# Performance work log

Hardware: AMD Instinct MI355X
Metric: run time of the kernel (lower is better)

## Reference

```python
import jax, jax.numpy as jnp
import numpy as np

N_NODES = 100000
N_EDGES = 1600000
N_GRAPHS = 512


def _graph_conv(x, W, b, src, dst, n_nodes):
    """DGL GraphConv, norm='both': D_in^-1/2 (A (D_out^-1/2 x)) W + b.
    Weight is applied on the smaller-dim side (same math, less memory)."""
    ones = jnp.ones(src.shape[0], dtype=x.dtype)
    deg_out = jnp.clip(jax.ops.segment_sum(ones, src, num_segments=n_nodes), 1.0)
    deg_in = jnp.clip(jax.ops.segment_sum(ones, dst, num_segments=n_nodes), 1.0)
    h = x * (deg_out ** -0.5)[:, None]
    if W.shape[0] > W.shape[1]:  # reduce feature dim before the SpMM
        h = h @ W
        h = jax.ops.segment_sum(h[src], dst, num_segments=n_nodes)
    else:
        h = jax.ops.segment_sum(h[src], dst, num_segments=n_nodes)
        h = h @ W
    return h * (deg_in ** -0.5)[:, None] + b


def setup_inputs() -> dict:
    key = jax.random.key(0)
    ks = jax.random.split(key, 16)
    x = jax.random.normal(ks[0], (N_NODES, 128), dtype=jnp.float32)
    src = jax.random.randint(ks[1], (N_EDGES,), 0, N_NODES, dtype=jnp.int32)
    dst = jax.random.randint(ks[2], (N_EDGES,), 0, N_NODES, dtype=jnp.int32)
    graph_ids = jnp.sort(jax.random.randint(ks[3], (N_NODES,), 0, N_GRAPHS, dtype=jnp.int32))
    s = 0.05
    return {
        "x": x, "src": src, "dst": dst, "graph_ids": graph_ids,
        "W1": jax.random.normal(ks[4], (128, 256), jnp.float32) * s,
        "b1": jnp.zeros((256,), jnp.float32),
        "W2": jax.random.normal(ks[5], (256, 64), jnp.float32) * s,
        "b2": jnp.zeros((64,), jnp.float32),
        "Wc1": jax.random.normal(ks[6], (64, 18), jnp.float32) * s,
        "bc1": jnp.zeros((18,), jnp.float32),
        "Wc2": jax.random.normal(ks[7], (18, 12), jnp.float32) * s,
        "bc2": jnp.zeros((12,), jnp.float32),
        "Wc3": jax.random.normal(ks[8], (12, 6), jnp.float32) * s,
        "bc3": jnp.zeros((6,), jnp.float32),
        "Wc4": jax.random.normal(ks[9], (6, 2), jnp.float32) * s,
        "bc4": jnp.zeros((2,), jnp.float32),
    }


def reference(x, src, dst, graph_ids, W1, b1, W2, b2, Wc1, bc1, Wc2, bc2, Wc3, bc3, Wc4, bc4):
    n = x.shape[0]
    h = jax.nn.relu(_graph_conv(x, W1, b1, src, dst, n))
    h = jax.nn.relu(_graph_conv(h, W2, b2, src, dst, n))
    # dgl.mean_nodes: per-graph mean over nodes
    sums = jax.ops.segment_sum(h, graph_ids, num_segments=N_GRAPHS)
    cnts = jnp.clip(jax.ops.segment_sum(jnp.ones(n, h.dtype), graph_ids, num_segments=N_GRAPHS), 1.0)
    hg = sums / cnts[:, None]
    # classifier: 4 stacked Linear layers, no activations (faithful to source)
    hg = hg @ Wc1 + bc1
    hg = hg @ Wc2 + bc2
    hg = hg @ Wc3 + bc3
    return hg @ Wc4 + bc4
```

## Files before the change

kernel.cpp:

```cpp
#include <hip/hip_runtime.h>
#include <cstdint>
#include <cstddef>

#define NGRAPHS 512

static inline size_t align_up(size_t x, size_t a){ return (x + a - 1) & ~(a - 1); }

__device__ __forceinline__ unsigned short f2bf(float f){
  unsigned int u = __float_as_uint(f);
  u += 0x7FFFu + ((u >> 16) & 1u);
  return (unsigned short)(u >> 16);
}
__device__ __forceinline__ float bflo(unsigned int u){ return __uint_as_float(u << 16); }
__device__ __forceinline__ float bfhi(unsigned int u){ return __uint_as_float(u & 0xffff0000u); }
__device__ __forceinline__ unsigned int pack2(float a, float b){
  return (unsigned)f2bf(a) | ((unsigned)f2bf(b) << 16);
}

typedef __attribute__((ext_vector_type(8))) short bf16x8;
typedef __attribute__((ext_vector_type(4))) float f32x4;

__global__ __launch_bounds__(256) void k_partcount(const int* __restrict__ src, const int* __restrict__ dst,
                                                   int* __restrict__ cntS, int* __restrict__ cntD, int n_edges, int NBLK,
                                                   const float* __restrict__ W1, unsigned short* __restrict__ Wt1,
                                                   const float* __restrict__ W2, unsigned short* __restrict__ Wt2,
                                                   const int* __restrict__ gids, int* __restrict__ gb, int n_nodes){
  __shared__ int cs[256], cd[256];
  if (blockIdx.x >= NBLK){
    long long u = (long long)(blockIdx.x - NBLK) * 256 + threadIdx.x;
    if (u < 128 * 256){
      int k = (int)(u / 256), n = (int)(u % 256);
      Wt1[(size_t)n * 128 + k] = f2bf(W1[u]);
      return;
    }
    u -= 128 * 256;
    if (u < 256 * 64){
      int k = (int)(u / 64), n = (int)(u % 64);
      Wt2[(size_t)n * 256 + k] = f2bf(W2[u]);
      return;
    }
    u -= 256 * 64;
    if (u < n_nodes){
      int i = (int)u;
      int g  = gids[i];
      int gp = (i > 0) ? gids[i - 1] : -1;
      for (int q = gp + 1; q <= g; ++q) gb[q] = i;
      if (i == n_nodes - 1)
        for (int q = g + 1; q <= NGRAPHS; ++q) gb[q] = n_nodes;
    }
    return;
  }
  int tid = threadIdx.x;
  cs[tid] = 0; cd[tid] = 0;
  __syncthreads();
  int e0 = blockIdx.x * 4096;
  int e1 = min(e0 + 4096, n_edges);
  for (int e = e0 + tid; e < e1; e += 256){
    atomicAdd(&cs[src[e] >> 9], 1);
    atomicAdd(&cd[dst[e] >> 9], 1);
  }
  __syncthreads();
  cntS[blockIdx.x * 256 + tid] = cs[tid];
  cntD[blockIdx.x * 256 + tid] = cd[tid];
}

__global__ __launch_bounds__(256) void k_colscan(int* __restrict__ cntS, int* __restrict__ cntD,
                                                 int* __restrict__ totS, int* __restrict__ totD,
                                                 int nblk, int NB){
  int col = blockIdx.x;
  int* cnt; int* tot; int k;
  if (col < NB){ cnt = cntS; tot = totS; k = col; }
  else         { cnt = cntD; tot = totD; k = col - NB; }
  __shared__ int tsum[256];
  int tid = threadIdx.x;
  int i0 = 2 * tid, i1 = 2 * tid + 1;
  int a = (i0 < nblk) ? cnt[i0 * 256 + k] : 0;
  int b = (i1 < nblk) ? cnt[i1 * 256 + k] : 0;
  int s = a + b;
  tsum[tid] = s;
  __syncthreads();
  for (int off = 1; off < 256; off <<= 1){
    int t = (tid >= off) ? tsum[tid - off] : 0;
    __syncthreads();
    tsum[tid] += t;
    __syncthreads();
  }
  int pre = tsum[tid] - s;
  if (i0 < nblk) cnt[i0 * 256 + k] = pre;
  if (i1 < nblk) cnt[i1 * 256 + k] = pre + a;
  if (tid == 255) tot[k] = tsum[255];
}

__global__ __launch_bounds__(256) void k_scatter_det(const int* __restrict__ src, const int* __restrict__ dst,
                                                     const int* __restrict__ cntS, const int* __restrict__ cntD,
                                                     const int* __restrict__ totS, const int* __restrict__ totD,
                                                     int* __restrict__ baseS, int* __restrict__ baseD,
                                                     int2* __restrict__ pairD, int* __restrict__ srcS,
                                                     int n_edges, int NB){
  __shared__ int s1[256], s2[256];
  __shared__ int gbS[256], gbD[256], lsS[256], lsD[256], lcS[256], lcD[256];
  __shared__ int2 ebuf[4096];
  __shared__ int sbuf[4096];
  int tid = threadIdx.x;
  int b = blockIdx.x;
  int v1 = (tid < NB) ? totS[tid] : 0;
  int v2 = (tid < NB) ? totD[tid] : 0;
  s1[tid] = v1; s2[tid] = v2;
  __syncthreads();
  for (int off = 1; off < 256; off <<= 1){
    int t1 = (tid >= off) ? s1[tid - off] : 0;
    int t2 = (tid >= off) ? s2[tid - off] : 0;
    __syncthreads();
    s1[tid] += t1; s2[tid] += t2;
    __syncthreads();
  }
  int bS = s1[tid] - v1, bD = s2[tid] - v2;
  if (b == 0 && tid < NB){ baseS[tid] = bS; baseD[tid] = bD; }
  gbS[tid] = bS + cntS[b * 256 + tid];
  gbD[tid] = bD + cntD[b * 256 + tid];
  __syncthreads();
  int e0 = b * 4096, e1 = min(e0 + 4096, n_edges);
  int ne = e1 - e0;
  s1[tid] = 0; s2[tid] = 0;
  __syncthreads();
  for (int e = e0 + tid; e < e1; e += 256){
    atomicAdd(&s1[src[e] >> 9], 1);
    atomicAdd(&s2[dst[e] >> 9], 1);
  }
  __syncthreads();
  int hv1 = s1[tid], hv2 = s2[tid];
  __syncthreads();
  s1[tid] = hv1; s2[tid] = hv2;
  __syncthreads();
  for (int off = 1; off < 256; off <<= 1){
    int t1 = (tid >= off) ? s1[tid - off] : 0;
    int t2 = (tid >= off) ? s2[tid - off] : 0;
    __syncthreads();
    s1[tid] += t1; s2[tid] += t2;
    __syncthreads();
  }
  lsS[tid] = s1[tid] - hv1; lcS[tid] = lsS[tid];
  lsD[tid] = s2[tid] - hv2; lcD[tid] = lsD[tid];
  __syncthreads();
  for (int e = e0 + tid; e < e1; e += 256){
    int sv = src[e], d = dst[e];
    int lp = atomicAdd(&lcD[d >> 9], 1);
    ebuf[lp] = make_int2(sv, d);
    int sp = atomicAdd(&lcS[sv >> 9], 1);
    sbuf[sp] = sv;
  }
  __syncthreads();
  for (int i = tid; i < ne; i += 256){
    int2 e = ebuf[i];
    int kd = e.y >> 9;
    pairD[gbD[kd] + i - lsD[kd]] = e;
    int sv = sbuf[i];
    int ks = sv >> 9;
    srcS[gbS[ks] + i - lsS[ks]] = sv;
  }
}

__global__ __launch_bounds__(256) void k_bucket_build(const int2* __restrict__ pairD, const int* __restrict__ baseD,
                                                      const int* __restrict__ srcS, const int* __restrict__ baseS,
                                                      int* __restrict__ offs, float* __restrict__ din_s,
                                                      float* __restrict__ dout_s, int* __restrict__ csr_src,
                                                      int NB, int n, int n_edges){
  __shared__ int cnt[512], cur[512];
  __shared__ int tsum[256];
  int tid = threadIdx.x;
  int bb = blockIdx.x;
  bool dstSide = bb < NB;
  int b = dstSide ? bb : bb - NB;
  int node0 = b << 9;
  int nn = min(512, n - node0);
  for (int i = tid; i < 512; i += 256) cnt[i] = 0;
  __syncthreads();
  if (dstSide){
    int jd0 = baseD[b], jd1 = (b + 1 < NB) ? baseD[b + 1] : n_edges;
    for (int j = jd0 + tid; j < jd1; j += 256) atomicAdd(&cnt[pairD[j].y - node0], 1);
    __syncthreads();
    int a0 = cnt[2 * tid], a1 = cnt[2 * tid + 1];
    int s = a0 + a1;
    tsum[tid] = s;
    __syncthreads();
    for (int off = 1; off < 256; off <<= 1){
      int t = (tid >= off) ? tsum[tid - off] : 0;
      __syncthreads();
      tsum[tid] += t;
      __syncthreads();
    }
    int pre = tsum[tid] - s + jd0;
    cur[2 * tid]     = pre;
    cur[2 * tid + 1] = pre + a0;
    __syncthreads();
    for (int i = tid; i < nn; i += 256){
      offs[node0 + i]  = cur[i];
      din_s[node0 + i] = 1.0f / sqrtf((float)max(cnt[i], 1));
    }
    if (b == NB - 1 && tid == 0) offs[n] = n_edges;
    __syncthreads();
    for (int j = jd0 + tid; j < jd1; j += 256){
      int2 e = pairD[j];
      int p = atomicAdd(&cur[e.y - node0], 1);
      csr_src[p] = e.x;
    }
  } else {
    int js0 = baseS[b], js1 = (b + 1 < NB) ? baseS[b + 1] : n_edges;
    for (int j = js0 + tid; j < js1; j += 256) atomicAdd(&cnt[srcS[j] - node0], 1);
    __syncthreads();
    for (int i = tid; i < nn; i += 256)
      dout_s[node0 + i] = 1.0f / sqrtf((float)max(cnt[i], 1));
  }
}

__global__ __launch_bounds__(256) void k_prep2(const float* __restrict__ x,
                                               const float* __restrict__ dout_s,
                                               unsigned int* __restrict__ xb, long long total4){
  long long t = (long long)blockIdx.x * 256 + threadIdx.x;
  if (t >= total4) return;
  float4 v = ((const float4*)x)[t];
  float s = dout_s[t >> 5];
  xb[t * 2 + 0] = pack2(v.x * s, v.y * s);
  xb[t * 2 + 1] = pack2(v.z * s, v.w * s);
}

__global__ __launch_bounds__(256) void k_spmm1(const unsigned int* __restrict__ xb,
    const int* __restrict__ offs, const int* __restrict__ csr_src,
    unsigned int* __restrict__ aggb, int n_nodes){
  int node = __builtin_amdgcn_readfirstlane((int)((blockIdx.x * 256u + threadIdx.x) >> 6));
  if (node >= n_nodes) return;
  int lane = threadIdx.x & 63;
  int j0 = offs[node], j1 = offs[node + 1];
  float ax = 0.f, ay = 0.f;
  int j = j0;
  for (; j + 4 <= j1; j += 4){
    int s0 = csr_src[j + 0];
    int s1 = csr_src[j + 1];
    int s2 = csr_src[j + 2];
    int s3 = csr_src[j + 3];
    unsigned v0 = xb[(size_t)s0 * 64 + lane];
    unsigned v1 = xb[(size_t)s1 * 64 + lane];
    unsigned v2 = xb[(size_t)s2 * 64 + lane];
    unsigned v3 = xb[(size_t)s3 * 64 + lane];
    ax += bflo(v0) + bflo(v1) + bflo(v2) + bflo(v3);
    ay += bfhi(v0) + bfhi(v1) + bfhi(v2) + bfhi(v3);
  }
  for (; j < j1; ++j){
    unsigned v = xb[(size_t)csr_src[j] * 64 + lane];
    ax += bflo(v);
    ay += bfhi(v);
  }
  aggb[(size_t)node * 64 + lane] = pack2(ax, ay);
}

__global__ __launch_bounds__(256) void k_gemm12(const unsigned short* __restrict__ A,
    const unsigned short* __restrict__ Bt, const unsigned short* __restrict__ Wt2,
    unsigned short* __restrict__ T2,
    int M, const float* __restrict__ din, const float* __restrict__ dout,
    const float* __restrict__ bias){
  constexpr int LDA = 136;
  constexpr int LDH = 72;
  __shared__ __align__(16) unsigned short As[128 * LDA];
  __shared__ __align__(16) unsigned short Bs[64 * LDA];
  __shared__ __align__(16) unsigned short Hs[128 * LDH];
  int tid = threadIdx.x;
  int bm0 = blockIdx.x * 128;
  int wid = tid >> 6, lane = tid & 63;
  int wm = wid * 32;
  int quad = lane >> 4, l16 = lane & 15;

  uint4 areg[8];
#pragma unroll
  for (int it = 0; it < 8; ++it){
    int i = tid + it * 256;
    int m = i >> 4, c = i & 15;
    int gr = bm0 + m;
    areg[it] = (gr < M) ? *(const uint4*)(A + (size_t)gr * 128 + c * 8) : make_uint4(0u, 0u, 0u, 0u);
  }
  uint4 breg[4];
#pragma unroll
  for (int it = 0; it < 4; ++it){
    int i = tid + it * 256;
    int n = i >> 4, c = i & 15;
    breg[it] = *(const uint4*)(Bt + (size_t)n * 128 + c * 8);
  }
#pragma unroll
  for (int it = 0; it < 8; ++it){
    int i = tid + it * 256;
    int m = i >> 4, c = i & 15;
    *(uint4*)&As[m * LDA + c * 8] = areg[it];
  }
#pragma unroll
  for (int it = 0; it < 4; ++it){
    int i = tid + it * 256;
    int n = i >> 4, c = i & 15;
    *(uint4*)&Bs[n * LDA + c * 8] = breg[it];
  }
  float rsv[2][4], rs2v[2][4];
#pragma unroll
  for (int t = 0; t < 2; ++t)
#pragma unroll
    for (int r = 0; r < 4; ++r){
      int gr = bm0 + wm + t * 16 + quad * 4 + r;
      rsv[t][r]  = (gr < M) ? din[gr]  : 0.f;
      rs2v[t][r] = (gr < M) ? dout[gr] : 0.f;
    }
  f32x4 tacc[2][4];
#pragma unroll
  for (int t = 0; t < 2; ++t)
#pragma unroll
    for (int u = 0; u < 4; ++u) tacc[t][u] = f32x4{0.f, 0.f, 0.f, 0.f};
  __syncthreads();

  for (int nt = 0; nt < 4; ++nt){
    if (nt < 3){
#pragma unroll
      for (int it = 0; it < 4; ++it){
        int i = tid + it * 256;
        int n = i >> 4, c = i & 15;
        breg[it] = *(const uint4*)(Bt + (size_t)((nt + 1) * 64 + n) * 128 + c * 8);
      }
    }
    f32x4 acc[2][4];
#pragma unroll
    for (int t = 0; t < 2; ++t)
#pragma unroll
      for (int u = 0; u < 4; ++u) acc[t][u] = f32x4{0.f, 0.f, 0.f, 0.f};
#pragma unroll
    for (int ks = 0; ks < 4; ++ks){
      bf16x8 af[2], bfr[4];
#pragma unroll
      for (int t = 0; t < 2; ++t)
        af[t] = *(const bf16x8*)&As[(wm + t * 16 + l16) * LDA + ks * 32 + quad * 8];
#pragma unroll
      for (int u = 0; u < 4; ++u)
        bfr[u] = *(const bf16x8*)&Bs[(u * 16 + l16) * LDA + ks * 32 + quad * 8];
#pragma unroll
      for (int t = 0; t < 2; ++t)
#pragma unroll
        for (int u = 0; u < 4; ++u)
          acc[t][u] = __builtin_amdgcn_mfma_f32_16x16x32_bf16(af[t], bfr[u], acc[t][u], 0, 0, 0);
    }
    float bv[4];
#pragma unroll
    for (int u = 0; u < 4; ++u) bv[u] = bias[nt * 64 + u * 16 + l16];
#pragma unroll
    for (int t = 0; t < 2; ++t)
#pragma unroll
      for (int r = 0; r < 4; ++r){
        int row = wm + t * 16 + quad * 4 + r;
#pragma unroll
        for (int u = 0; u < 4; ++u){
          float cv = fmaxf(fmaf(acc[t][u][r], rsv[t][r], bv[u]), 0.f) * rs2v[t][r];
          Hs[row * LDH + u * 16 + l16] = f2bf(cv);
        }
      }
    __syncthreads();
#pragma unroll
    for (int ks2 = 0; ks2 < 2; ++ks2){
      bf16x8 haf[2], wbf[4];
#pragma unroll
      for (int t = 0; t < 2; ++t)
        haf[t] = *(const bf16x8*)&Hs[(wm + t * 16 + l16) * LDH + ks2 * 32 + quad * 8];
#pragma unroll
      for (int u = 0; u < 4; ++u)
        wbf[u] = *(const bf16x8*)(Wt2 + (size_t)(u * 16 + l16) * 256 + nt * 64 + ks2 * 32 + quad * 8);
#pragma unroll
      for (int t = 0; t < 2; ++t)
#pragma unroll
        for (int u = 0; u < 4; ++u)
          tacc[t][u] = __builtin_amdgcn_mfma_f32_16x16x32_bf16(haf[t], wbf[u], tacc[t][u], 0, 0, 0);
    }
    __syncthreads();
    if (nt < 3){
#pragma unroll
      for (int it = 0; it < 4; ++it){
        int i = tid + it * 256;
        int n = i >> 4, c = i & 15;
        *(uint4*)&Bs[n * LDA + c * 8] = breg[it];
      }
      __syncthreads();
    }
  }
#pragma unroll
  for (int t = 0; t < 2; ++t)
#pragma unroll
    for (int r = 0; r < 4; ++r){
      int gr = bm0 + wm + t * 16 + quad * 4 + r;
      if (gr < M){
#pragma unroll
        for (int u = 0; u < 4; ++u)
          T2[(size_t)gr * 64 + u * 16 + l16] = f2bf(tacc[t][u][r]);
      }
    }
}

#define SCHUNK 4
__global__ __launch_bounds__(256) void k_spmm2_fused(const unsigned short* __restrict__ t2,
    const int* __restrict__ offs, const int* __restrict__ csr_src,
    const float* __restrict__ din_s, const float* __restrict__ b2,
    const int* __restrict__ gb, float* __restrict__ sums){
  __shared__ float bs[64];
  int tid = threadIdx.x;
  int g = blockIdx.x & (NGRAPHS - 1);
  int chunk = blockIdx.x >> 9;
  int wW = __builtin_amdgcn_readfirstlane(chunk * 4 + (tid >> 6));
  int lane = tid & 63, half = lane >> 5, l = lane & 31;
  if (tid < 64) bs[tid] = 0.f;
  __syncthreads();
  int g0 = gb[g], g1 = gb[g + 1];
  const unsigned int* tp = (const unsigned int*)t2;
  float2 bb = ((const float2*)b2)[l];
  float gxs = 0.f, gys = 0.f;
  for (int node = g0 + wW; node < g1; node += 16){
    int j0 = offs[node], j1 = offs[node + 1];
    float ax = 0.f, ay = 0.f;
    int j = j0;
    for (; j + 2 <= j1; j += 2){
      int s0 = csr_src[j], s1 = csr_src[j + 1];
      int ss = half ? s1 : s0;
      unsigned v = tp[(size_t)ss * 32 + l];
      ax += bflo(v);
      ay += bfhi(v);
    }
    if (j < j1 && half == 0){
      unsigned v = tp[(size_t)csr_src[j] * 32 + l];
      ax += bflo(v);
      ay += bfhi(v);
    }
    ax += __shfl_xor(ax, 32);
    ay += __shfl_xor(ay, 32);
    float ds = din_s[node];
    gxs += fmaxf(fmaf(ax, ds, bb.x), 0.f);
    gys += fmaxf(fmaf(ay, ds, bb.y), 0.f);
  }
  if (half == 0){
    atomicAdd(&bs[2 * l], gxs);
    atomicAdd(&bs[2 * l + 1], gys);
  }
  __syncthreads();
  if (tid < 64) atomicAdd(&sums[(size_t)g * 64 + tid], bs[tid]);
}

__global__ __launch_bounds__(256) void k_classifier(const float* __restrict__ sums, const int* __restrict__ gb,
    const float* __restrict__ Wc1, const float* __restrict__ bc1,
    const float* __restrict__ Wc2, const float* __restrict__ bc2,
    const float* __restrict__ Wc3, const float* __restrict__ bc3,
    const float* __restrict__ Wc4, const float* __restrict__ bc4,
    float* __restrict__ out){
  __shared__ float w1[64 * 18], w2[18 * 12], w3[12 * 6], w4[6 * 2];
  __shared__ float B1[18], B2[12], B3[6], B4[2];
  int tid = threadIdx.x;
  for (int i = tid; i < 64 * 18; i += 256) w1[i] = Wc1[i];
  for (int i = tid; i < 18 * 12; i += 256) w2[i] = Wc2[i];
  for (int i = tid; i < 12 * 6;  i += 256) w3[i] = Wc3[i];
  for (int i = tid; i < 6 * 2;   i += 256) w4[i] = Wc4[i];
  if (tid < 18) B1[tid] = bc1[tid];
  if (tid < 12) B2[tid] = bc2[tid];
  if (tid < 6)  B3[tid] = bc3[tid];
  if (tid < 2)  B4[tid] = bc4[tid];
  __syncthreads();
  int g = blockIdx.x * 256 + tid;
  float cnt = fmaxf((float)(gb[g + 1] - gb[g]), 1.0f);
  float h[64];
#pragma unroll
  for (int f = 0; f < 64; ++f) h[f] = sums[(size_t)g * 64 + f] / cnt;
  float t1[18];
#pragma unroll
  for (int j = 0; j < 18; ++j){
    float s = B1[j];
    for (int f = 0; f < 64; ++f) s = fmaf(h[f], w1[f * 18 + j], s);
    t1[j] = s;
  }
  float t2[12];
#pragma unroll
  for (int j = 0; j < 12; ++j){
    float s = B2[j];
    for (int f = 0; f < 18; ++f) s = fmaf(t1[f], w2[f * 12 + j], s);
    t2[j] = s;
  }
  float t3[6];
#pragma unroll
  for (int j = 0; j < 6; ++j){
    float s = B3[j];
    for (int f = 0; f < 12; ++f) s = fmaf(t2[f], w3[f * 6 + j], s);
    t3[j] = s;
  }
#pragma unroll
  for (int j = 0; j < 2; ++j){
    float s = B4[j];
    for (int f = 0; f < 6; ++f) s = fmaf(t3[f], w4[f * 2 + j], s);
    out[(size_t)g * 2 + j] = s;
  }
}

extern "C" void kernel_launch(void* const* d_in, const int* in_sizes, int n_in,
                              void* d_out, int out_size, void* d_ws, size_t ws_size,
                              hipStream_t stream){
  const float* x   = (const float*)d_in[0];
  const int*   src = (const int*)d_in[1];
  const int*   dst = (const int*)d_in[2];
  const int*   gid = (const int*)d_in[3];
  const float* W1  = (const float*)d_in[4];
  const float* b1  = (const float*)d_in[5];
  const float* W2  = (const float*)d_in[6];
  const float* b2  = (const float*)d_in[7];
  const float* Wc1 = (const float*)d_in[8];
  const float* bc1 = (const float*)d_in[9];
  const float* Wc2 = (const float*)d_in[10];
  const float* bc2 = (const float*)d_in[11];
  const float* Wc3 = (const float*)d_in[12];
  const float* bc3 = (const float*)d_in[13];
  const float* Wc4 = (const float*)d_in[14];
  const float* bc4 = (const float*)d_in[15];
  float* out = (float*)d_out;

  const int n_nodes = in_sizes[3];
  const int n_edges = in_sizes[1];
  const int F1 = 256, F2 = 64;
  const int NB   = (n_nodes + 511) >> 9;
  const int NBLK = (n_edges + 4095) / 4096;

  char* w = (char*)d_ws;
  size_t o = 0;
  auto alloc = [&](size_t bytes) -> char* {
    char* p = w + o;
    o = align_up(o + bytes, 256);
    return p;
  };
  float* sums      = (float*)alloc((size_t)NGRAPHS * F2 * 4);
  int*   gb        = (int*)  alloc((size_t)(NGRAPHS + 1) * 4);
  int*   cntS      = (int*)  alloc((size_t)NBLK * 256 * 4);
  int*   cntD      = (int*)  alloc((size_t)NBLK * 256 * 4);
  int*   totS      = (int*)  alloc((size_t)256 * 4);
  int*   totD      = (int*)  alloc((size_t)256 * 4);
  int*   baseS     = (int*)  alloc((size_t)256 * 4);
  int*   baseD     = (int*)  alloc((size_t)256 * 4);
  float* dout_s    = (float*)alloc((size_t)n_nodes * 4);
  float* din_s     = (float*)alloc((size_t)n_nodes * 4);
  int*   offs      = (int*)  alloc((size_t)(n_nodes + 1) * 4);
  int*   csr_src   = (int*)  alloc((size_t)n_edges * 4);
  unsigned short* Wt1 = (unsigned short*)alloc((size_t)256 * 128 * 2);
  unsigned short* Wt2 = (unsigned short*)alloc((size_t)64 * 256 * 2);
  unsigned int*   xb  = (unsigned int*)  alloc((size_t)n_nodes * 128 * 2);
  unsigned short* aggb= (unsigned short*)alloc((size_t)n_nodes * 128 * 2);
  unsigned short* h1b = (unsigned short*)alloc((size_t)n_nodes * F1 * 2);
  int2*  pairD = (int2*)aggb;
  int*   srcS  = (int*)((char*)aggb + (size_t)n_edges * 8);
  unsigned short* t2b = h1b;

  hipMemsetAsync(sums, 0, (size_t)NGRAPHS * F2 * 4, stream);

  {
    long long miscTotal = 128 * 256 + 256 * 64 + n_nodes;
    int miscBlocks = (int)((miscTotal + 255) / 256);
    k_partcount<<<NBLK + miscBlocks, 256, 0, stream>>>(src, dst, cntS, cntD, n_edges, NBLK,
                                                       W1, Wt1, W2, Wt2, gid, gb, n_nodes);
  }
  k_colscan     <<<2 * NB, 256, 0, stream>>>(cntS, cntD, totS, totD, NBLK, NB);
  k_scatter_det <<<NBLK, 256, 0, stream>>>(src, dst, cntS, cntD, totS, totD, baseS, baseD, pairD, srcS, n_edges, NB);
  k_bucket_build<<<2 * NB, 256, 0, stream>>>(pairD, baseD, srcS, baseS, offs, din_s, dout_s, csr_src,
                                             NB, n_nodes, n_edges);

  {
    long long total4 = (long long)n_nodes * 32;
    k_prep2<<<(int)((total4 + 255) / 256), 256, 0, stream>>>(x, dout_s, xb, total4);
  }

  int gx = (n_nodes + 127) / 128;
  {
    long long threads = (long long)n_nodes * 64;
    k_spmm1<<<(int)((threads + 255) / 256), 256, 0, stream>>>(xb, offs, csr_src, (unsigned int*)aggb, n_nodes);
    k_gemm12<<<gx, 256, 0, stream>>>(aggb, Wt1, Wt2, t2b, n_nodes, din_s, dout_s, b1);
  }
  k_spmm2_fused<<<NGRAPHS * SCHUNK, 256, 0, stream>>>(t2b, offs, csr_src, din_s, b2, gb, sums);
  k_classifier<<<NGRAPHS / 256, 256, 0, stream>>>(sums, gb, Wc1, bc1, Wc2, bc2, Wc3, bc3, Wc4, bc4, out);
}
```

Before: 345.2 us.

## Fuse layer-1 SpMM gather into the GEMM kernel and unroll layer-2 gather

The layer-1 neighbor aggregation now runs inside the GEMM kernel. Each wave gathers its own 32 rows, two nodes interleaved, straight into LDS, so the aggregated bf16 intermediate is never written to or re-read from global memory. The W1 tile is no longer staged in LDS; MFMA B fragments are read directly from global memory, which removes most block barriers. Layer-2 gather loops are unrolled to 8 edges for more memory-level parallelism. The tradeoff is only 782 blocks doing the irregular gather, so latency hiding may be worse, and repeated global reads of the weights add traffic.

```diff
diff --git a/kernel.cpp b/kernel.cpp
--- a/kernel.cpp
+++ b/kernel.cpp
@@ -224,44 +224,26 @@
   xb[t * 2 + 1] = pack2(v.z * s, v.w * s);
 }
 
-__global__ __launch_bounds__(256) void k_spmm1(const unsigned int* __restrict__ xb,
+__device__ __forceinline__ void gath4(const unsigned int* __restrict__ xb, const int* __restrict__ cs,
+                                      int j, int lane, float &ax, float &ay){
+  int s0 = cs[j], s1 = cs[j + 1], s2 = cs[j + 2], s3 = cs[j + 3];
+  unsigned v0 = xb[(size_t)s0 * 64 + lane];
+  unsigned v1 = xb[(size_t)s1 * 64 + lane];
+  unsigned v2 = xb[(size_t)s2 * 64 + lane];
+  unsigned v3 = xb[(size_t)s3 * 64 + lane];
+  ax += bflo(v0) + bflo(v1) + bflo(v2) + bflo(v3);
+  ay += bfhi(v0) + bfhi(v1) + bfhi(v2) + bfhi(v3);
+}
+
+__global__ __launch_bounds__(256) void k_spmmgemm(const unsigned int* __restrict__ xb,
     const int* __restrict__ offs, const int* __restrict__ csr_src,
-    unsigned int* __restrict__ aggb, int n_nodes){
-  int node = __builtin_amdgcn_readfirstlane((int)((blockIdx.x * 256u + threadIdx.x) >> 6));
-  if (node >= n_nodes) return;
-  int lane = threadIdx.x & 63;
-  int j0 = offs[node], j1 = offs[node + 1];
-  float ax = 0.f, ay = 0.f;
-  int j = j0;
-  for (; j + 4 <= j1; j += 4){
-    int s0 = csr_src[j + 0];
-    int s1 = csr_src[j + 1];
-    int s2 = csr_src[j + 2];
-    int s3 = csr_src[j + 3];
-    unsigned v0 = xb[(size_t)s0 * 64 + lane];
-    unsigned v1 = xb[(size_t)s1 * 64 + lane];
-    unsigned v2 = xb[(size_t)s2 * 64 + lane];
-    unsigned v3 = xb[(size_t)s3 * 64 + lane];
-    ax += bflo(v0) + bflo(v1) + bflo(v2) + bflo(v3);
-    ay += bfhi(v0) + bfhi(v1) + bfhi(v2) + bfhi(v3);
-  }
-  for (; j < j1; ++j){
-    unsigned v = xb[(size_t)csr_src[j] * 64 + lane];
-    ax += bflo(v);
-    ay += bfhi(v);
-  }
-  aggb[(size_t)node * 64 + lane] = pack2(ax, ay);
-}
-
-__global__ __launch_bounds__(256) void k_gemm12(const unsigned short* __restrict__ A,
-    const unsigned short* __restrict__ Bt, const unsigned short* __restrict__ Wt2,
+    const unsigned short* __restrict__ Wt1, const unsigned short* __restrict__ Wt2,
     unsigned short* __restrict__ T2,
     int M, const float* __restrict__ din, const float* __restrict__ dout,
     const float* __restrict__ bias){
   constexpr int LDA = 136;
   constexpr int LDH = 72;
   __shared__ __align__(16) unsigned short As[128 * LDA];
-  __shared__ __align__(16) unsigned short Bs[64 * LDA];
   __shared__ __align__(16) unsigned short Hs[128 * LDH];
   int tid = threadIdx.x;
   int bm0 = blockIdx.x * 128;
@@ -269,33 +251,45 @@
   int wm = wid * 32;
   int quad = lane >> 4, l16 = lane & 15;
 
-  uint4 areg[8];
-#pragma unroll
-  for (int it = 0; it < 8; ++it){
-    int i = tid + it * 256;
-    int m = i >> 4, c = i & 15;
-    int gr = bm0 + m;
-    areg[it] = (gr < M) ? *(const uint4*)(A + (size_t)gr * 128 + c * 8) : make_uint4(0u, 0u, 0u, 0u);
-  }
-  uint4 breg[4];
-#pragma unroll
-  for (int it = 0; it < 4; ++it){
-    int i = tid + it * 256;
-    int n = i >> 4, c = i & 15;
-    breg[it] = *(const uint4*)(Bt + (size_t)n * 128 + c * 8);
-  }
-#pragma unroll
-  for (int it = 0; it < 8; ++it){
-    int i = tid + it * 256;
-    int m = i >> 4, c = i & 15;
-    *(uint4*)&As[m * LDA + c * 8] = areg[it];
-  }
-#pragma unroll
-  for (int it = 0; it < 4; ++it){
-    int i = tid + it * 256;
-    int n = i >> 4, c = i & 15;
-    *(uint4*)&Bs[n * LDA + c * 8] = breg[it];
-  }
+  unsigned int* Asw = (unsigned int*)As;
+  for (int i = 0; i < 16; ++i){
+    int mA = wm + 2 * i, mB = mA + 1;
+    int gA = bm0 + mA, gB = bm0 + mB;
+    float axA = 0.f, ayA = 0.f, axB = 0.f, ayB = 0.f;
+    if (gB < M){
+      int ja = offs[gA], ja1 = offs[gA + 1];
+      int jb = offs[gB], jb1 = offs[gB + 1];
+      for (; ja + 4 <= ja1 && jb + 4 <= jb1; ja += 4, jb += 4){
+        gath4(xb, csr_src, ja, lane, axA, ayA);
+        gath4(xb, csr_src, jb, lane, axB, ayB);
+      }
+      for (; ja + 4 <= ja1; ja += 4) gath4(xb, csr_src, ja, lane, axA, ayA);
+      for (; ja < ja1; ++ja){
+        unsigned v = xb[(size_t)csr_src[ja] * 64 + lane];
+        axA += bflo(v); ayA += bfhi(v);
+      }
+      for (; jb + 4 <= jb1; jb += 4) gath4(xb, csr_src, jb, lane, axB, ayB);
+      for (; jb < jb1; ++jb){
+        unsigned v = xb[(size_t)csr_src[jb] * 64 + lane];
+        axB += bflo(v); ayB += bfhi(v);
+      }
+    } else if (gA < M){
+      int ja = offs[gA], ja1 = offs[gA + 1];
+      for (; ja + 8 <= ja1; ja += 8){
+        gath4(xb, csr_src, ja, lane, axA, ayA);
+        gath4(xb, csr_src, ja + 4, lane, axB, ayB);
+      }
+      for (; ja + 4 <= ja1; ja += 4) gath4(xb, csr_src, ja, lane, axA, ayA);
+      for (; ja < ja1; ++ja){
+        unsigned v = xb[(size_t)csr_src[ja] * 64 + lane];
+        axA += bflo(v); ayA += bfhi(v);
+      }
+      axA += axB; ayA += ayB; axB = 0.f; ayB = 0.f;
+    }
+    Asw[(size_t)mA * (LDA / 2) + lane] = pack2(axA, ayA);
+    Asw[(size_t)mB * (LDA / 2) + lane] = pack2(axB, ayB);
+  }
+
   float rsv[2][4], rs2v[2][4];
 #pragma unroll
   for (int t = 0; t < 2; ++t)
@@ -310,17 +304,8 @@
   for (int t = 0; t < 2; ++t)
 #pragma unroll
     for (int u = 0; u < 4; ++u) tacc[t][u] = f32x4{0.f, 0.f, 0.f, 0.f};
-  __syncthreads();
 
   for (int nt = 0; nt < 4; ++nt){
-    if (nt < 3){
-#pragma unroll
-      for (int it = 0; it < 4; ++it){
-        int i = tid + it * 256;
-        int n = i >> 4, c = i & 15;
-        breg[it] = *(const uint4*)(Bt + (size_t)((nt + 1) * 64 + n) * 128 + c * 8);
-      }
-    }
     f32x4 acc[2][4];
 #pragma unroll
     for (int t = 0; t < 2; ++t)
@@ -334,7 +319,7 @@
         af[t] = *(const bf16x8*)&As[(wm + t * 16 + l16) * LDA + ks * 32 + quad * 8];
 #pragma unroll
       for (int u = 0; u < 4; ++u)
-        bfr[u] = *(const bf16x8*)&Bs[(u * 16 + l16) * LDA + ks * 32 + quad * 8];
+        bfr[u] = *(const bf16x8*)(Wt1 + (size_t)(nt * 64 + u * 16 + l16) * 128 + ks * 32 + quad * 8);
 #pragma unroll
       for (int t = 0; t < 2; ++t)
 #pragma unroll
@@ -355,7 +340,6 @@
           Hs[row * LDH + u * 16 + l16] = f2bf(cv);
         }
       }
-    __syncthreads();
 #pragma unroll
     for (int ks2 = 0; ks2 < 2; ++ks2){
       bf16x8 haf[2], wbf[4];
@@ -370,16 +354,6 @@
 #pragma unroll
         for (int u = 0; u < 4; ++u)
           tacc[t][u] = __builtin_amdgcn_mfma_f32_16x16x32_bf16(haf[t], wbf[u], tacc[t][u], 0, 0, 0);
-    }
-    __syncthreads();
-    if (nt < 3){
-#pragma unroll
-      for (int it = 0; it < 4; ++it){
-        int i = tid + it * 256;
-        int n = i >> 4, c = i & 15;
-        *(uint4*)&Bs[n * LDA + c * 8] = breg[it];
-      }
-      __syncthreads();
     }
   }
 #pragma unroll
@@ -416,6 +390,32 @@
     int j0 = offs[node], j1 = offs[node + 1];
     float ax = 0.f, ay = 0.f;
     int j = j0;
+    for (; j + 8 <= j1; j += 8){
+      int s0 = csr_src[j + 0];
+      int s1 = csr_src[j + 1];
+      int s2 = csr_src[j + 2];
+      int s3 = csr_src[j + 3];
+      int s4 = csr_src[j + 4];
+      int s5 = csr_src[j + 5];
+      int s6 = csr_src[j + 6];
+      int s7 = csr_src[j + 7];
+      unsigned va = tp[(size_t)(half ? s1 : s0) * 32 + l];
+      unsigned vb = tp[(size_t)(half ? s3 : s2) * 32 + l];
+      unsigned vc = tp[(size_t)(half ? s5 : s4) * 32 + l];
+      unsigned vd = tp[(size_t)(half ? s7 : s6) * 32 + l];
+      ax += bflo(va) + bflo(vb) + bflo(vc) + bflo(vd);
+      ay += bfhi(va) + bfhi(vb) + bfhi(vc) + bfhi(vd);
+    }
+    for (; j + 4 <= j1; j += 4){
+      int s0 = csr_src[j + 0];
+      int s1 = csr_src[j + 1];
+      int s2 = csr_src[j + 2];
+      int s3 = csr_src[j + 3];
+      unsigned va = tp[(size_t)(half ? s1 : s0) * 32 + l];
+      unsigned vb = tp[(size_t)(half ? s3 : s2) * 32 + l];
+      ax += bflo(va) + bflo(vb);
+      ay += bfhi(va) + bfhi(vb);
+    }
     for (; j + 2 <= j1; j += 2){
       int s0 = csr_src[j], s1 = csr_src[j + 1];
       int ss = half ? s1 : s0;
@@ -568,11 +568,8 @@
   }
 
   int gx = (n_nodes + 127) / 128;
-  {
-    long long threads = (long long)n_nodes * 64;
-    k_spmm1<<<(int)((threads + 255) / 256), 256, 0, stream>>>(xb, offs, csr_src, (unsigned int*)aggb, n_nodes);
-    k_gemm12<<<gx, 256, 0, stream>>>(aggb, Wt1, Wt2, t2b, n_nodes, din_s, dout_s, b1);
-  }
+  k_spmmgemm<<<gx, 256, 0, stream>>>(xb, offs, csr_src, Wt1, Wt2, t2b,
+                                     n_nodes, din_s, dout_s, b1);
   k_spmm2_fused<<<NGRAPHS * SCHUNK, 256, 0, stream>>>(t2b, offs, csr_src, din_s, b2, gb, sums);
   k_classifier<<<NGRAPHS / 256, 256, 0, stream>>>(sums, gb, Wc1, bc1, Wc2, bc2, Wc3, bc3, Wc4, bc4, out);
 }
```

Result: slower. 419.8 us (+21.6%).
